# Optimization experiments

Measured on AMD Instinct MI355X. Metric: run time of the kernel, lower is better.

Reference implementation:

```python
import jax, jax.numpy as jnp
import numpy as np

B, G, S, H = 4, 8, 1024, 1024
KD = H // 8  # key_dim = hidden_dim // 8


def setup_inputs() -> dict:
    key = jax.random.key(0)
    ks = jax.random.split(key, 8)
    x = jax.random.normal(ks[0], (B, G, S, H), dtype=jnp.float32)
    inv_h = 1.0 / np.sqrt(H).astype(np.float32)
    Wq = jax.random.normal(ks[1], (H, KD), dtype=jnp.float32) * inv_h
    bq = jax.random.normal(ks[2], (KD,), dtype=jnp.float32) * 0.01
    Wk = jax.random.normal(ks[3], (H, KD), dtype=jnp.float32) * inv_h
    bk = jax.random.normal(ks[4], (KD,), dtype=jnp.float32) * 0.01
    Wv = jax.random.normal(ks[5], (H, H), dtype=jnp.float32) * inv_h
    bv = jax.random.normal(ks[6], (H,), dtype=jnp.float32) * 0.01
    gamma = jax.random.normal(ks[7], (1,), dtype=jnp.float32) * 0.1
    return {"x": x, "Wq": Wq, "bq": bq, "Wk": Wk, "bk": bk, "Wv": Wv, "bv": bv, "gamma": gamma}


def reference(x, Wq, bq, Wk, bk, Wv, bv, gamma):
    # x: [b, g, q, f]
    q = x @ Wq + bq          # [b, g, q, kd]
    k = x @ Wk + bk          # [b, g, k, kd]
    v = x @ Wv + bv          # [b, g, v, f]
    # NOTE: original forward never applies self.scale -> unscaled logits.
    att = jax.nn.softmax(jnp.einsum('bgqf,bgkf->bgqk', q, k), axis=-1)
    out = jnp.einsum('bgvf,bgqv->bgqf', v, att)
    return gamma * out + x
```

## Files before the change

### kernel.cpp

```cpp
#include <hip/hip_runtime.h>

typedef unsigned short u16;
typedef unsigned char u8;
typedef __attribute__((ext_vector_type(8))) short bf16x8;
typedef __attribute__((ext_vector_type(4))) float f32x4;

__device__ __forceinline__ u16 f2bf(float f) {
  unsigned u = __builtin_bit_cast(unsigned, f);
  u += 0x7fffu + ((u >> 16) & 1u);
  return (u16)(u >> 16);
}

__device__ __forceinline__ float bf2f(u16 h) {
  unsigned u = ((unsigned)h) << 16;
  return __builtin_bit_cast(float, u);
}

__device__ __forceinline__ unsigned pkbf(float lo, float hi) {
  unsigned r;
  asm("v_cvt_pk_bf16_f32 %0, %1, %2" : "=v"(r) : "v"(lo), "v"(hi));
  return r;
}

__device__ __forceinline__ void gll16(const void* g, void* l) {
  __builtin_amdgcn_global_load_lds((const __attribute__((address_space(1))) void*)g,
                                   (__attribute__((address_space(3))) void*)l, 16, 0, 0);
}

__global__ void prep_k(const float* __restrict__ x, u16* __restrict__ xb,
                       const float* __restrict__ Wq, const float* __restrict__ Wk,
                       const float* __restrict__ Wv, u16* __restrict__ wt,
                       const float* __restrict__ bq, const float* __restrict__ bk,
                       const float* __restrict__ bv, float* __restrict__ bc) {
  __shared__ float tile[64][65];
  const int b = blockIdx.x;
  const int t = threadIdx.x;
  if (b < 16384) {
    const size_t i = ((size_t)b * 256 + t) * 8;
    float4 a = *(const float4*)(x + i);
    float4 c = *(const float4*)(x + i + 4);
    uint4 u;
    u.x = pkbf(a.x, a.y);
    u.y = pkbf(a.z, a.w);
    u.z = pkbf(c.x, c.y);
    u.w = pkbf(c.z, c.w);
    *(uint4*)(xb + i) = u;
  } else if (b < 16704) {
    const int tb = b - 16384;
    const int n0 = (tb % 20) * 64;
    const int f0 = (tb / 20) * 64;
    const float* src; int ld, coff;
    if (n0 < 128)      { src = Wq; ld = 128;  coff = n0; }
    else if (n0 < 256) { src = Wk; ld = 128;  coff = n0 - 128; }
    else               { src = Wv; ld = 1024; coff = n0 - 256; }
    const int r = t >> 4, c4 = (t & 15) * 4;
    #pragma unroll
    for (int i = 0; i < 4; ++i) {
      float4 v = *(const float4*)(src + (size_t)(f0 + r + 16 * i) * ld + coff + c4);
      tile[r + 16 * i][c4 + 0] = v.x;
      tile[r + 16 * i][c4 + 1] = v.y;
      tile[r + 16 * i][c4 + 2] = v.z;
      tile[r + 16 * i][c4 + 3] = v.w;
    }
    __syncthreads();
    #pragma unroll
    for (int i = 0; i < 4; ++i) {
      const int nr = r + 16 * i;
      ushort4 h;
      h.x = f2bf(tile[c4 + 0][nr]);
      h.y = f2bf(tile[c4 + 1][nr]);
      h.z = f2bf(tile[c4 + 2][nr]);
      h.w = f2bf(tile[c4 + 3][nr]);
      *(ushort4*)(wt + (size_t)(n0 + nr) * 1024 + f0 + c4) = h;
    }
  } else {
    for (int i = t; i < 1280; i += 256)
      bc[i] = (i < 128) ? bq[i] : ((i < 256) ? bk[i - 128] : bv[i - 256]);
  }
}

__global__ __launch_bounds__(256, 2) void gemm_qkv_k(
    const u16* __restrict__ xb, const u16* __restrict__ wt,
    const float* __restrict__ bc, u16* __restrict__ qkv, u8* __restrict__ vt) {
  __shared__ u16 sA[128 * 64];
  __shared__ u16 sB[128 * 64];
  char* sAc = (char*)sA;
  char* sBc = (char*)sB;
  const int t = threadIdx.x;
  const int w = t >> 6, lane = t & 63;
  const int wr = w >> 1, wc = w & 1;
  const int lm = lane & 15, lg = lane >> 4;
  const int bid = blockIdx.x;
  const int xcd = bid & 7, g = bid >> 3;
  const int mb = xcd + 8 * (g / 10);
  const int nt = g % 10;
  const int m0 = mb * 128;
  const int n0 = nt * 128;
  const f32x4 FZ = {0.f, 0.f, 0.f, 0.f};

  const int brow = t >> 3;
  const int bcol = 8 * ((t & 7) ^ ((t >> 3) & 7));
  const int kswz = (lm & 7) << 4;
  const u16* ab = xb + (size_t)(m0 + brow) * 1024 + bcol;
  const u16* wb = wt + (size_t)(n0 + brow) * 1024 + bcol;

  f32x4 acc[4][4];
  #pragma unroll
  for (int mi = 0; mi < 4; ++mi)
    #pragma unroll
    for (int ni = 0; ni < 4; ++ni) acc[mi][ni] = FZ;

  for (int kt = 0; kt < 16; ++kt) {
    const int k0 = kt * 64;
    char* da = sAc + w * 1024;
    char* db = sBc + w * 1024;
    #pragma unroll
    for (int i = 0; i < 4; ++i) {
      gll16(ab + (size_t)(32 * i) * 1024 + k0, da + 4096 * i);
      gll16(wb + (size_t)(32 * i) * 1024 + k0, db + 4096 * i);
    }
    __syncthreads();
    #pragma unroll
    for (int ks = 0; ks < 2; ++ks) {
      const int ka = (ks * 64 + lg * 16) ^ kswz;
      bf16x8 aF[4], bF[4];
      #pragma unroll
      for (int mi = 0; mi < 4; ++mi)
        aF[mi] = *(const bf16x8*)(sAc + (wr * 64 + mi * 16 + lm) * 128 + ka);
      #pragma unroll
      for (int ni = 0; ni < 4; ++ni)
        bF[ni] = *(const bf16x8*)(sBc + (wc * 64 + ni * 16 + lm) * 128 + ka);
      #pragma unroll
      for (int mi = 0; mi < 4; ++mi)
        #pragma unroll
        for (int ni = 0; ni < 4; ++ni)
          acc[mi][ni] = __builtin_amdgcn_mfma_f32_16x16x32_bf16(aF[mi], bF[ni], acc[mi][ni], 0, 0, 0);
    }
    __syncthreads();
  }

  if (n0 < 256) {
    #pragma unroll
    for (int ni = 0; ni < 4; ++ni) {
      const int col = n0 + wc * 64 + ni * 16 + lm;
      const float bias = bc[col];
      #pragma unroll
      for (int mi = 0; mi < 4; ++mi) {
        const int r0 = m0 + wr * 64 + mi * 16 + lg * 4;
        #pragma unroll
        for (int j = 0; j < 4; ++j)
          qkv[(size_t)(r0 + j) * 256 + col] = f2bf(acc[mi][ni][j] + bias);
      }
    }
  } else {
    #pragma unroll
    for (int ni = 0; ni < 4; ++ni) {
      const int col = n0 + wc * 64 + ni * 16 + lm;
      const float bias = bc[col];
      const int h = col - 256;
      #pragma unroll
      for (int mi = 0; mi < 4; ++mi) {
        const int r0 = m0 + wr * 64 + mi * 16 + lg * 4;
        const int bg = r0 >> 10;
        const int sb = r0 & 1023;
        unsigned v32 = __builtin_amdgcn_cvt_pk_fp8_f32(acc[mi][ni][0] + bias,
                                                       acc[mi][ni][1] + bias, 0, false);
        v32 = __builtin_amdgcn_cvt_pk_fp8_f32(acc[mi][ni][2] + bias,
                                              acc[mi][ni][3] + bias, v32, true);
        *(unsigned*)(vt + ((size_t)(bg * 1024 + h) << 10) + sb) = v32;
      }
    }
  }
}

__global__ __launch_bounds__(512, 2) void qks_k(const u16* __restrict__ qk,
                                                u8* __restrict__ P) {
  __shared__ float smax[8][32];
  __shared__ float ssum[8][32];
  const int t = threadIdx.x;
  const int w = t >> 6, lane = t & 63;
  const int lm = lane & 15, lg = lane >> 4;
  const int bid = blockIdx.x;
  const int qt = (bid >> 3) & 31;
  const int bg = (((bid >> 8) & 3) << 3) | (bid & 7);
  const f32x4 FZ = {0.f, 0.f, 0.f, 0.f};

  bf16x8 qf[2][4];
  #pragma unroll
  for (int qc = 0; qc < 2; ++qc)
    #pragma unroll
    for (int ks = 0; ks < 4; ++ks)
      qf[qc][ks] = *(const bf16x8*)(qk +
          (size_t)(bg * 1024 + qt * 32 + qc * 16 + lm) * 256 + ks * 32 + lg * 8);

  f32x4 sc[8][2];
  #pragma unroll
  for (int ch = 0; ch < 8; ++ch) { sc[ch][0] = FZ; sc[ch][1] = FZ; }
  const u16* kbase = qk + (size_t)(bg * 1024 + w * 128) * 256 + 128;
  #pragma unroll
  for (int ch = 0; ch < 8; ++ch) {
    bf16x8 kf[4];
    #pragma unroll
    for (int ks = 0; ks < 4; ++ks)
      kf[ks] = *(const bf16x8*)(kbase + (size_t)(ch * 16 + lm) * 256 + ks * 32 + lg * 8);
    #pragma unroll
    for (int ks = 0; ks < 4; ++ks) {
      sc[ch][0] = __builtin_amdgcn_mfma_f32_16x16x32_bf16(kf[ks], qf[0][ks], sc[ch][0], 0, 0, 0);
      sc[ch][1] = __builtin_amdgcn_mfma_f32_16x16x32_bf16(kf[ks], qf[1][ks], sc[ch][1], 0, 0, 0);
    }
  }

  float mx[2];
  #pragma unroll
  for (int qc = 0; qc < 2; ++qc) {
    float m = sc[0][qc][0];
    #pragma unroll
    for (int ch = 0; ch < 8; ++ch)
      #pragma unroll
      for (int j = 0; j < 4; ++j) m = fmaxf(m, sc[ch][qc][j]);
    m = fmaxf(m, __shfl_xor(m, 16));
    m = fmaxf(m, __shfl_xor(m, 32));
    mx[qc] = m;
  }
  if (lg == 0) { smax[w][lm] = mx[0]; smax[w][16 + lm] = mx[1]; }
  __syncthreads();
  float gm[2];
  #pragma unroll
  for (int qc = 0; qc < 2; ++qc) {
    float m = smax[0][qc * 16 + lm];
    #pragma unroll
    for (int wp = 1; wp < 8; ++wp) m = fmaxf(m, smax[wp][qc * 16 + lm]);
    gm[qc] = m;
  }

  float ls[2] = {0.f, 0.f};
  #pragma unroll
  for (int ch = 0; ch < 8; ++ch)
    #pragma unroll
    for (int qc = 0; qc < 2; ++qc) {
      f32x4 e;
      #pragma unroll
      for (int j = 0; j < 4; ++j) e[j] = __expf(sc[ch][qc][j] - gm[qc]);
      sc[ch][qc] = e;
      ls[qc] += (e[0] + e[1]) + (e[2] + e[3]);
    }
  #pragma unroll
  for (int qc = 0; qc < 2; ++qc) {
    ls[qc] += __shfl_xor(ls[qc], 16);
    ls[qc] += __shfl_xor(ls[qc], 32);
  }
  if (lg == 0) { ssum[w][lm] = ls[0]; ssum[w][16 + lm] = ls[1]; }
  __syncthreads();
  float inv[2];
  #pragma unroll
  for (int qc = 0; qc < 2; ++qc) {
    float s = ssum[0][qc * 16 + lm];
    #pragma unroll
    for (int wp = 1; wp < 8; ++wp) s += ssum[wp][qc * 16 + lm];
    inv[qc] = 1.0f / s;
  }

  const int s0 = (2 * (lg & 1)) * 16 + lm;
  const int s1 = s0 + 16;
  const bool lo = (lg < 2);
  #pragma unroll
  for (int qc = 0; qc < 2; ++qc) {
    u8* pr = P + ((size_t)(bg * 1024 + qt * 32 + qc * 16 + lm) << 10) + w * 128 + lg * 8;
    #pragma unroll
    for (int c = 0; c < 4; ++c) {
      unsigned ue = __builtin_amdgcn_cvt_pk_fp8_f32(sc[2 * c][qc][0] * inv[qc],
                                                    sc[2 * c][qc][1] * inv[qc], 0, false);
      ue = __builtin_amdgcn_cvt_pk_fp8_f32(sc[2 * c][qc][2] * inv[qc],
                                           sc[2 * c][qc][3] * inv[qc], ue, true);
      unsigned uo = __builtin_amdgcn_cvt_pk_fp8_f32(sc[2 * c + 1][qc][0] * inv[qc],
                                                    sc[2 * c + 1][qc][1] * inv[qc], 0, false);
      uo = __builtin_amdgcn_cvt_pk_fp8_f32(sc[2 * c + 1][qc][2] * inv[qc],
                                           sc[2 * c + 1][qc][3] * inv[qc], uo, true);
      unsigned e0 = __shfl(ue, s0), o0 = __shfl(uo, s0);
      unsigned e1 = __shfl(ue, s1), o1 = __shfl(uo, s1);
      uint2 pw;
      pw.x = lo ? e0 : o0;
      pw.y = lo ? e1 : o1;
      *(uint2*)(pr + c * 32) = pw;
    }
  }
}

__global__ __launch_bounds__(256, 2) void pv_k(
    const u8* __restrict__ P, const u8* __restrict__ vt,
    const u16* __restrict__ xb, const float* __restrict__ gam,
    float* __restrict__ out) {
  __shared__ u8 sA[128 * 128];
  __shared__ u8 sB[128 * 128];
  char* sAc = (char*)sA;
  char* sBc = (char*)sB;
  const int t = threadIdx.x;
  const int w = t >> 6, lane = t & 63;
  const int wr = w >> 1, wc = w & 1;
  const int lm = lane & 15, lg = lane >> 4;
  const int bid = blockIdx.x;
  const int bg = (((bid >> 9) & 3) << 3) | (bid & 7);
  const int qb = (bid >> 6) & 7;
  const int hb = (bid >> 3) & 7;
  const int m0 = qb * 128, n0 = hb * 128;
  const f32x4 FZ = {0.f, 0.f, 0.f, 0.f};

  const int brow = t >> 3;
  const int bcol = 16 * ((t & 7) ^ ((t >> 3) & 7));
  const int kswz = (lm & 7) << 4;
  const u8* pb = P + ((size_t)(bg * 1024 + m0 + brow) << 10) + bcol;
  const u8* wb = vt + ((size_t)(bg * 1024 + n0 + brow) << 10) + bcol;

  f32x4 acc[4][4];
  #pragma unroll
  for (int mi = 0; mi < 4; ++mi)
    #pragma unroll
    for (int ni = 0; ni < 4; ++ni) acc[mi][ni] = FZ;

  for (int kt = 0; kt < 8; ++kt) {
    const int k0 = kt * 128;
    #pragma unroll
    for (int i = 0; i < 4; ++i) {
      gll16(pb + (size_t)(32 * i) * 1024 + k0, sAc + i * 4096 + t * 16);
      gll16(wb + (size_t)(32 * i) * 1024 + k0, sBc + i * 4096 + t * 16);
    }
    __syncthreads();
    #pragma unroll
    for (int ks = 0; ks < 4; ++ks) {
      const int ka = (ks * 32 + lg * 8) ^ kswz;
      long aF[4], bF[4];
      #pragma unroll
      for (int mi = 0; mi < 4; ++mi)
        aF[mi] = *(const long*)(sAc + (wr * 64 + mi * 16 + lm) * 128 + ka);
      #pragma unroll
      for (int ni = 0; ni < 4; ++ni)
        bF[ni] = *(const long*)(sBc + (wc * 64 + ni * 16 + lm) * 128 + ka);
      #pragma unroll
      for (int mi = 0; mi < 4; ++mi)
        #pragma unroll
        for (int ni = 0; ni < 4; ++ni)
          acc[mi][ni] = __builtin_amdgcn_mfma_f32_16x16x32_fp8_fp8(aF[mi], bF[ni], acc[mi][ni], 0, 0, 0);
    }
    __syncthreads();
  }

  const float g0 = gam[0];
  #pragma unroll
  for (int mi = 0; mi < 4; ++mi)
    #pragma unroll
    for (int j = 0; j < 4; ++j) {
      const size_t row = (size_t)(bg * 1024 + m0 + wr * 64 + mi * 16 + lg * 4 + j);
      #pragma unroll
      for (int ni = 0; ni < 4; ++ni) {
        const int col = n0 + wc * 64 + ni * 16 + lm;
        const size_t idx = row * 1024 + col;
        __builtin_nontemporal_store(g0 * acc[mi][ni][j] + bf2f(xb[idx]), &out[idx]);
      }
    }
}

extern "C" void kernel_launch(void* const* d_in, const int* in_sizes, int n_in,
                              void* d_out, int out_size, void* d_ws, size_t ws_size,
                              hipStream_t stream) {
  const float* x  = (const float*)d_in[0];
  const float* Wq = (const float*)d_in[1];
  const float* bq = (const float*)d_in[2];
  const float* Wk = (const float*)d_in[3];
  const float* bk = (const float*)d_in[4];
  const float* Wv = (const float*)d_in[5];
  const float* bv = (const float*)d_in[6];
  const float* gm = (const float*)d_in[7];
  float* out = (float*)d_out;

  char* ws = (char*)d_ws;
  u16*   wt = (u16*)(ws);
  float* bc = (float*)(ws + 2621440);
  u16*   qk = (u16*)(ws + 2626560);
  u8*    vt = (u8*)(ws + 19403776);
  u8*    Pm = (u8*)(ws + 52958208);
  u16*   xb = (u16*)(ws + 86512640);

  prep_k<<<16705, 256, 0, stream>>>(x, xb, Wq, Wk, Wv, wt, bq, bk, bv, bc);
  gemm_qkv_k<<<dim3(2560), 256, 0, stream>>>(xb, wt, bc, qk, vt);
  qks_k<<<dim3(1024), 512, 0, stream>>>(qk, Pm);
  pv_k<<<dim3(2048), 256, 0, stream>>>(Pm, vt, xb, gm, out);
}
```

Baseline: 227.8 us.

## Split QKV GEMM and compute V projection with FP8 MFMA

The fused QKV projection GEMM is split in two. Q/K stays in bf16, and the V projection becomes a separate FP8 GEMM using mfma_f32_16x16x32_fp8_fp8. The prep kernel now also writes FP8 copies of x and Wv, which adds extra global writes (about 32 MB more for x). The aim is to roughly double matrix throughput and halve operand bytes for the dominant 1024x1024 V projection. This lowers V precision further, since its inputs are now quantized to FP8 as well as its output.

```diff
diff --git a/kernel.cpp b/kernel.cpp
--- a/kernel.cpp
+++ b/kernel.cpp
@@ -27,9 +27,9 @@
                                    (__attribute__((address_space(3))) void*)l, 16, 0, 0);
 }
 
-__global__ void prep_k(const float* __restrict__ x, u16* __restrict__ xb,
+__global__ void prep_k(const float* __restrict__ x, u16* __restrict__ xb, u8* __restrict__ xf8,
                        const float* __restrict__ Wq, const float* __restrict__ Wk,
-                       const float* __restrict__ Wv, u16* __restrict__ wt,
+                       const float* __restrict__ Wv, u16* __restrict__ wt, u8* __restrict__ wv8,
                        const float* __restrict__ bq, const float* __restrict__ bk,
                        const float* __restrict__ bv, float* __restrict__ bc) {
   __shared__ float tile[64][65];
@@ -45,6 +45,13 @@
     u.z = pkbf(c.x, c.y);
     u.w = pkbf(c.z, c.w);
     *(uint4*)(xb + i) = u;
+    uint2 v;
+    unsigned p0 = __builtin_amdgcn_cvt_pk_fp8_f32(a.x, a.y, 0, false);
+    p0 = __builtin_amdgcn_cvt_pk_fp8_f32(a.z, a.w, p0, true);
+    unsigned p1 = __builtin_amdgcn_cvt_pk_fp8_f32(c.x, c.y, 0, false);
+    p1 = __builtin_amdgcn_cvt_pk_fp8_f32(c.z, c.w, p1, true);
+    v.x = p0; v.y = p1;
+    *(uint2*)(xf8 + i) = v;
   } else if (b < 16704) {
     const int tb = b - 16384;
     const int n0 = (tb % 20) * 64;
@@ -63,15 +70,25 @@
       tile[r + 16 * i][c4 + 3] = v.w;
     }
     __syncthreads();
-    #pragma unroll
-    for (int i = 0; i < 4; ++i) {
-      const int nr = r + 16 * i;
-      ushort4 h;
-      h.x = f2bf(tile[c4 + 0][nr]);
-      h.y = f2bf(tile[c4 + 1][nr]);
-      h.z = f2bf(tile[c4 + 2][nr]);
-      h.w = f2bf(tile[c4 + 3][nr]);
-      *(ushort4*)(wt + (size_t)(n0 + nr) * 1024 + f0 + c4) = h;
+    if (n0 < 256) {
+      #pragma unroll
+      for (int i = 0; i < 4; ++i) {
+        const int nr = r + 16 * i;
+        ushort4 h;
+        h.x = f2bf(tile[c4 + 0][nr]);
+        h.y = f2bf(tile[c4 + 1][nr]);
+        h.z = f2bf(tile[c4 + 2][nr]);
+        h.w = f2bf(tile[c4 + 3][nr]);
+        *(ushort4*)(wt + (size_t)(n0 + nr) * 1024 + f0 + c4) = h;
+      }
+    } else {
+      #pragma unroll
+      for (int i = 0; i < 4; ++i) {
+        const int nr = r + 16 * i;
+        unsigned v8 = __builtin_amdgcn_cvt_pk_fp8_f32(tile[c4 + 0][nr], tile[c4 + 1][nr], 0, false);
+        v8 = __builtin_amdgcn_cvt_pk_fp8_f32(tile[c4 + 2][nr], tile[c4 + 3][nr], v8, true);
+        *(unsigned*)(wv8 + (size_t)(n0 - 256 + nr) * 1024 + f0 + c4) = v8;
+      }
     }
   } else {
     for (int i = t; i < 1280; i += 256)
@@ -79,9 +96,9 @@
   }
 }
 
-__global__ __launch_bounds__(256, 2) void gemm_qkv_k(
+__global__ __launch_bounds__(256, 2) void gemm_qk_k(
     const u16* __restrict__ xb, const u16* __restrict__ wt,
-    const float* __restrict__ bc, u16* __restrict__ qkv, u8* __restrict__ vt) {
+    const float* __restrict__ bc, u16* __restrict__ qkv) {
   __shared__ u16 sA[128 * 64];
   __shared__ u16 sB[128 * 64];
   char* sAc = (char*)sA;
@@ -92,8 +109,8 @@
   const int lm = lane & 15, lg = lane >> 4;
   const int bid = blockIdx.x;
   const int xcd = bid & 7, g = bid >> 3;
-  const int mb = xcd + 8 * (g / 10);
-  const int nt = g % 10;
+  const int mb = xcd + 8 * (g >> 1);
+  const int nt = g & 1;
   const int m0 = mb * 128;
   const int n0 = nt * 128;
   const f32x4 FZ = {0.f, 0.f, 0.f, 0.f};
@@ -139,36 +156,92 @@
     __syncthreads();
   }
 
-  if (n0 < 256) {
-    #pragma unroll
-    for (int ni = 0; ni < 4; ++ni) {
-      const int col = n0 + wc * 64 + ni * 16 + lm;
-      const float bias = bc[col];
-      #pragma unroll
-      for (int mi = 0; mi < 4; ++mi) {
-        const int r0 = m0 + wr * 64 + mi * 16 + lg * 4;
+  #pragma unroll
+  for (int ni = 0; ni < 4; ++ni) {
+    const int col = n0 + wc * 64 + ni * 16 + lm;
+    const float bias = bc[col];
+    #pragma unroll
+    for (int mi = 0; mi < 4; ++mi) {
+      const int r0 = m0 + wr * 64 + mi * 16 + lg * 4;
+      #pragma unroll
+      for (int j = 0; j < 4; ++j)
+        qkv[(size_t)(r0 + j) * 256 + col] = f2bf(acc[mi][ni][j] + bias);
+    }
+  }
+}
+
+__global__ __launch_bounds__(256, 2) void gemm_v_k(
+    const u8* __restrict__ xf8, const u8* __restrict__ wv8,
+    const float* __restrict__ bc, u8* __restrict__ vt) {
+  __shared__ u8 sA[128 * 128];
+  __shared__ u8 sB[128 * 128];
+  char* sAc = (char*)sA;
+  char* sBc = (char*)sB;
+  const int t = threadIdx.x;
+  const int w = t >> 6, lane = t & 63;
+  const int wr = w >> 1, wc = w & 1;
+  const int lm = lane & 15, lg = lane >> 4;
+  const int bid = blockIdx.x;
+  const int xcd = bid & 7, g = bid >> 3;
+  const int mb = xcd + 8 * (g >> 3);
+  const int nt = g & 7;
+  const int m0 = mb * 128;
+  const int n0 = nt * 128;
+  const f32x4 FZ = {0.f, 0.f, 0.f, 0.f};
+
+  const int brow = t >> 3;
+  const int bcol = 16 * ((t & 7) ^ ((t >> 3) & 7));
+  const int kswz = (lm & 7) << 4;
+  const u8* ab = xf8 + (size_t)(m0 + brow) * 1024 + bcol;
+  const u8* wb = wv8 + (size_t)(n0 + brow) * 1024 + bcol;
+
+  f32x4 acc[4][4];
+  #pragma unroll
+  for (int mi = 0; mi < 4; ++mi)
+    #pragma unroll
+    for (int ni = 0; ni < 4; ++ni) acc[mi][ni] = FZ;
+
+  for (int kt = 0; kt < 8; ++kt) {
+    const int k0 = kt * 128;
+    #pragma unroll
+    for (int i = 0; i < 4; ++i) {
+      gll16(ab + (size_t)(32 * i) * 1024 + k0, sAc + i * 4096 + t * 16);
+      gll16(wb + (size_t)(32 * i) * 1024 + k0, sBc + i * 4096 + t * 16);
+    }
+    __syncthreads();
+    #pragma unroll
+    for (int ks = 0; ks < 4; ++ks) {
+      const int ka = (ks * 32 + lg * 8) ^ kswz;
+      long aF[4], bF[4];
+      #pragma unroll
+      for (int mi = 0; mi < 4; ++mi)
+        aF[mi] = *(const long*)(sAc + (wr * 64 + mi * 16 + lm) * 128 + ka);
+      #pragma unroll
+      for (int ni = 0; ni < 4; ++ni)
+        bF[ni] = *(const long*)(sBc + (wc * 64 + ni * 16 + lm) * 128 + ka);
+      #pragma unroll
+      for (int mi = 0; mi < 4; ++mi)
         #pragma unroll
-        for (int j = 0; j < 4; ++j)
-          qkv[(size_t)(r0 + j) * 256 + col] = f2bf(acc[mi][ni][j] + bias);
-      }
-    }
-  } else {
-    #pragma unroll
-    for (int ni = 0; ni < 4; ++ni) {
-      const int col = n0 + wc * 64 + ni * 16 + lm;
-      const float bias = bc[col];
-      const int h = col - 256;
-      #pragma unroll
-      for (int mi = 0; mi < 4; ++mi) {
-        const int r0 = m0 + wr * 64 + mi * 16 + lg * 4;
-        const int bg = r0 >> 10;
-        const int sb = r0 & 1023;
-        unsigned v32 = __builtin_amdgcn_cvt_pk_fp8_f32(acc[mi][ni][0] + bias,
-                                                       acc[mi][ni][1] + bias, 0, false);
-        v32 = __builtin_amdgcn_cvt_pk_fp8_f32(acc[mi][ni][2] + bias,
-                                              acc[mi][ni][3] + bias, v32, true);
-        *(unsigned*)(vt + ((size_t)(bg * 1024 + h) << 10) + sb) = v32;
-      }
+        for (int ni = 0; ni < 4; ++ni)
+          acc[mi][ni] = __builtin_amdgcn_mfma_f32_16x16x32_fp8_fp8(aF[mi], bF[ni], acc[mi][ni], 0, 0, 0);
+    }
+    __syncthreads();
+  }
+
+  #pragma unroll
+  for (int ni = 0; ni < 4; ++ni) {
+    const int h = n0 + wc * 64 + ni * 16 + lm;
+    const float bias = bc[256 + h];
+    #pragma unroll
+    for (int mi = 0; mi < 4; ++mi) {
+      const int r0 = m0 + wr * 64 + mi * 16 + lg * 4;
+      const int bg = r0 >> 10;
+      const int sb = r0 & 1023;
+      unsigned v32 = __builtin_amdgcn_cvt_pk_fp8_f32(acc[mi][ni][0] + bias,
+                                                     acc[mi][ni][1] + bias, 0, false);
+      v32 = __builtin_amdgcn_cvt_pk_fp8_f32(acc[mi][ni][2] + bias,
+                                            acc[mi][ni][3] + bias, v32, true);
+      *(unsigned*)(vt + ((size_t)(bg * 1024 + h) << 10) + sb) = v32;
     }
   }
 }
@@ -373,15 +446,18 @@
   float* out = (float*)d_out;
 
   char* ws = (char*)d_ws;
-  u16*   wt = (u16*)(ws);
-  float* bc = (float*)(ws + 2621440);
-  u16*   qk = (u16*)(ws + 2626560);
-  u8*    vt = (u8*)(ws + 19403776);
-  u8*    Pm = (u8*)(ws + 52958208);
-  u16*   xb = (u16*)(ws + 86512640);
-
-  prep_k<<<16705, 256, 0, stream>>>(x, xb, Wq, Wk, Wv, wt, bq, bk, bv, bc);
-  gemm_qkv_k<<<dim3(2560), 256, 0, stream>>>(xb, wt, bc, qk, vt);
+  u16*   wt  = (u16*)(ws);
+  float* bc  = (float*)(ws + 524288);
+  u16*   qk  = (u16*)(ws + 529408);
+  u8*    vt  = (u8*)(ws + 17306624);
+  u8*    Pm  = (u8*)(ws + 50861056);
+  u16*   xb  = (u16*)(ws + 84415488);
+  u8*    xf8 = (u8*)(ws + 151524352);
+  u8*    wv8 = (u8*)(ws + 185078784);
+
+  prep_k<<<16705, 256, 0, stream>>>(x, xb, xf8, Wq, Wk, Wv, wt, wv8, bq, bk, bv, bc);
+  gemm_qk_k<<<dim3(512), 256, 0, stream>>>(xb, wt, bc, qk);
+  gemm_v_k<<<dim3(2048), 256, 0, stream>>>(xf8, wv8, bc, vt);
   qks_k<<<dim3(1024), 512, 0, stream>>>(qk, Pm);
   pv_k<<<dim3(2048), 256, 0, stream>>>(Pm, vt, xb, gm, out);
 }
```

Result: no change. 228.7 us (+0.4%).
